# Kernel tuning notes

Measured on AMD Instinct MI355X. Metric: run time of the kernel, lower is better.

## Reference

```python
import jax, jax.numpy as jnp
import numpy as np

B, HW, C, D = 8, 65536, 64, 64  # batch, seq (H*W), channels, d_model
H = W = 256


def setup_inputs() -> dict:
    key = jax.random.key(0)
    ks = jax.random.split(key, 16)
    s = lambda k, shape, scale=0.05: jax.random.normal(k, shape, dtype=jnp.float32) * scale
    return {
        "x": jax.random.normal(ks[0], (B, HW, C), dtype=jnp.float32),
        "freq_map": jax.random.uniform(ks[1], (B, 1, H, W), dtype=jnp.float32),
        # proj_in: Linear(C, D)
        "W_in": s(ks[2], (C, D)), "b_in": s(ks[3], (D,)),
        # SimplifiedMambaKernel: in_proj Linear(D, 2D)
        "W_ip": s(ks[4], (D, 2 * D)), "b_ip": s(ks[5], (2 * D,)),
        # depthwise Conv1d(D, D, k=3, padding=1, groups=D): weight [D,1,3]
        "conv_w": s(ks[6], (D, 1, 3)), "conv_b": s(ks[7], (D,)),
        # mamba out_proj Linear(D, D)
        "W_op": s(ks[8], (D, D)), "b_op": s(ks[9], (D,)),
        # gate_net: Linear(1,16) -> ReLU -> Linear(16,C) -> Sigmoid
        "W_g1": s(ks[10], (1, 16)), "b_g1": s(ks[11], (16,)),
        "W_g2": s(ks[12], (16, C)), "b_g2": s(ks[13], (C,)),
        # proj_out: Linear(D, C)
        "W_out": s(ks[14], (D, C)), "b_out": s(ks[15], (C,)),
    }


def _mamba_kernel(feat, W_ip, b_ip, conv_w, conv_b, W_op, b_op):
    # feat: [B, L, D]
    x_and_res = feat @ W_ip + b_ip                      # [B, L, 2D]
    x_branch, res_branch = jnp.split(x_and_res, 2, axis=-1)
    xb = jnp.transpose(x_branch, (0, 2, 1))             # [B, D, L]
    xb = jax.lax.conv_general_dilated(
        xb, conv_w, window_strides=(1,), padding=[(1, 1)],
        feature_group_count=conv_w.shape[0],
        dimension_numbers=("NCH", "OIH", "NCH"))
    xb = xb + conv_b[None, :, None]
    x_branch = jnp.transpose(xb, (0, 2, 1))             # [B, L, D]
    out = jax.nn.silu(x_branch) * jax.nn.silu(res_branch)
    return out @ W_op + b_op


def reference(x, freq_map, W_in, b_in, W_ip, b_ip, conv_w, conv_b,
              W_op, b_op, W_g1, b_g1, W_g2, b_g2, W_out, b_out):
    feat = x @ W_in + b_in                              # [B, L, D]
    feat = _mamba_kernel(feat, W_ip, b_ip, conv_w, conv_b, W_op, b_op)
    feat_out = feat @ W_out + b_out                     # [B, L, C]
    # freq_map [B,1,H,W] -> flatten(2).permute(0,2,1) -> [B, L, 1]
    freq_flat = freq_map.reshape(freq_map.shape[0], 1, -1).transpose(0, 2, 1)
    gate = jax.nn.sigmoid(jax.nn.relu(freq_flat @ W_g1 + b_g1) @ W_g2 + b_g2)
    return feat_out * gate
```

## Files before the change

### kernel.cpp

```cpp
#include <hip/hip_runtime.h>
#include <hip/hip_bf16.h>

#define L_SEQ 65536
#define TILE 64
#define TILES_PER_B 1024

typedef __attribute__((ext_vector_type(8))) short bf16x8;
typedef __attribute__((ext_vector_type(4))) short s16x4;
typedef __attribute__((ext_vector_type(4))) float f32x4;

#define WS_WFX   0
#define WS_W1R   24576
#define WS_W2T   32768
#define WS_WG2T  40960
#define WS_BX    43008
#define WS_BR    43264
#define WS_BC0   43520
#define WS_BC2   43776
#define WS_B2    44032

__device__ __forceinline__ short f2bf(float f) {
    __bf16 h = (__bf16)f;
    return __builtin_bit_cast(short, h);
}
__device__ __forceinline__ float fsigmoid(float x) {
    return __builtin_amdgcn_rcpf(1.0f + __builtin_amdgcn_exp2f(-1.44269504089f * x));
}

__global__ void prep_kernel(const float* __restrict__ W_in, const float* __restrict__ b_in,
                            const float* __restrict__ W_ip, const float* __restrict__ b_ip,
                            const float* __restrict__ conv_w, const float* __restrict__ conv_b,
                            const float* __restrict__ W_op, const float* __restrict__ b_op,
                            const float* __restrict__ W_g2,
                            const float* __restrict__ W_out, const float* __restrict__ b_out,
                            void* __restrict__ ws)
{
    short* wfx  = (short*)((char*)ws + WS_WFX);
    short* w1r  = (short*)((char*)ws + WS_W1R);
    short* w2t  = (short*)((char*)ws + WS_W2T);
    short* wg2t = (short*)((char*)ws + WS_WG2T);
    float* bx   = (float*)((char*)ws + WS_BX);
    float* br   = (float*)((char*)ws + WS_BR);
    float* bc0  = (float*)((char*)ws + WS_BC0);
    float* bc2  = (float*)((char*)ws + WS_BC2);
    float* b2   = (float*)((char*)ws + WS_B2);

    int tid = blockIdx.x * blockDim.x + threadIdx.x;
    if (tid < 12288) {
        int s = tid >> 12, rem = tid & 4095;
        int d = rem >> 6, c = rem & 63;
        float acc = 0.f;
        for (int e = 0; e < 64; ++e) acc += W_in[c*64 + e] * W_ip[e*128 + d];
        wfx[(s*64 + d)*64 + c] = f2bf(acc * conv_w[3*d + s]);
    } else if (tid < 16384) {
        int rem = tid - 12288; int d = rem >> 6, c = rem & 63;
        float acc = 0.f;
        for (int e = 0; e < 64; ++e) acc += W_in[c*64 + e] * W_ip[e*128 + 64 + d];
        w1r[d*64 + c] = f2bf(acc);
    } else if (tid < 20480) {
        int rem = tid - 16384; int cp = rem >> 6, d = rem & 63;
        float acc = 0.f;
        for (int e = 0; e < 64; ++e) acc += W_op[d*64 + e] * W_out[e*64 + cp];
        w2t[cp*64 + d] = f2bf(acc);
    } else if (tid < 21504) {
        int rem = tid - 20480; int c = rem >> 4, j = rem & 15;
        wg2t[c*16 + j] = f2bf(W_g2[j*64 + c]);
    } else if (tid < 21568) {
        int d = tid - 21504;
        float b1x = b_ip[d];
        for (int e = 0; e < 64; ++e) b1x += b_in[e] * W_ip[e*128 + d];
        bx[d] = b1x * (conv_w[3*d] + conv_w[3*d+1] + conv_w[3*d+2]) + conv_b[d];
    } else if (tid < 21632) {
        int d = tid - 21568;
        float s = b_ip[64 + d];
        for (int e = 0; e < 64; ++e) s += b_in[e] * W_ip[e*128 + 64 + d];
        br[d] = s;
    } else if (tid < 21696) {
        int d = tid - 21632;
        float b1x = b_ip[d];
        for (int e = 0; e < 64; ++e) b1x += b_in[e] * W_ip[e*128 + d];
        bc0[d] = b1x * conv_w[3*d];
    } else if (tid < 21760) {
        int d = tid - 21696;
        float b1x = b_ip[d];
        for (int e = 0; e < 64; ++e) b1x += b_in[e] * W_ip[e*128 + d];
        bc2[d] = b1x * conv_w[3*d + 2];
    } else if (tid < 21824) {
        int cp = tid - 21760;
        float s = b_out[cp];
        for (int e = 0; e < 64; ++e) s += b_op[e] * W_out[e*64 + cp];
        b2[cp] = s;
    }
}

__global__ __launch_bounds__(256, 6) void fgs_main(
    const float* __restrict__ x, const float* __restrict__ freq,
    const float* __restrict__ wg1, const float* __restrict__ bg1,
    const float* __restrict__ bg2,
    const void* __restrict__ ws, float* __restrict__ out)
{
    const short* wfx  = (const short*)((const char*)ws + WS_WFX);
    const short* w1r  = (const short*)((const char*)ws + WS_W1R);
    const short* w2t  = (const short*)((const char*)ws + WS_W2T);
    const short* wg2t = (const short*)((const char*)ws + WS_WG2T);
    const float* bxv  = (const float*)((const char*)ws + WS_BX);
    const float* brv  = (const float*)((const char*)ws + WS_BR);
    const float* bc0  = (const float*)((const char*)ws + WS_BC0);
    const float* bc2  = (const float*)((const char*)ws + WS_BC2);
    const float* b2   = (const float*)((const char*)ws + WS_B2);

    __shared__ short xs[66 * 64];
    __shared__ short ot[64][72];
    __shared__ short hl[64][16];

    const int bid   = blockIdx.x;
    const int batch = bid >> 10;
    const int tile  = bid & 1023;
    const int base  = tile << 6;
    const bool edge = (tile == 0) || (tile == 1023);

    const int lane = threadIdx.x & 63;
    const int w    = threadIdx.x >> 6;
    const int lr   = lane & 15;
    const int g    = lane >> 4;
    const int r    = 16*w + lr;

    const size_t brow0 = (size_t)batch * L_SEQ;

    {
        auto stage_row = [&](int i, int cf) {
            int grow = base - 1 + i;
            bool v = ((unsigned)grow < (unsigned)L_SEQ);
            const float* p = x + (brow0 + (size_t)(v ? grow : 0)) * 64 + cf;
            float4 a = *(const float4*)(p);
            float4 b = *(const float4*)(p + 4);
            float4 c = *(const float4*)(p + 8);
            float4 d = *(const float4*)(p + 12);
            bf16x8 lo, hi;
            lo[0]=f2bf(a.x); lo[1]=f2bf(a.y); lo[2]=f2bf(a.z); lo[3]=f2bf(a.w);
            lo[4]=f2bf(b.x); lo[5]=f2bf(b.y); lo[6]=f2bf(b.z); lo[7]=f2bf(b.w);
            hi[0]=f2bf(c.x); hi[1]=f2bf(c.y); hi[2]=f2bf(c.z); hi[3]=f2bf(c.w);
            hi[4]=f2bf(d.x); hi[5]=f2bf(d.y); hi[6]=f2bf(d.z); hi[7]=f2bf(d.w);
            if (!v) { bf16x8 z = {}; lo = z; hi = z; }
            int c0 = cf >> 3;
            int sw = i & 7;
            *(bf16x8*)&xs[i*64 + ((c0    ) ^ sw) * 8] = lo;
            *(bf16x8*)&xs[i*64 + ((c0 + 1) ^ sw) * 8] = hi;
        };
        stage_row(threadIdx.x >> 2, (threadIdx.x & 3) * 16);
        if (threadIdx.x < 8)
            stage_row(64 + (threadIdx.x >> 2), (threadIdx.x & 3) * 16);
    }

    if (g < 2) {
        float f = freq[brow0 + base + r];
        float4 wa = *(const float4*)(wg1 + 8*g);
        float4 wb = *(const float4*)(wg1 + 8*g + 4);
        float4 ba = *(const float4*)(bg1 + 8*g);
        float4 bb = *(const float4*)(bg1 + 8*g + 4);
        bf16x8 hv;
        hv[0] = f2bf(fmaxf(f*wa.x + ba.x, 0.f));
        hv[1] = f2bf(fmaxf(f*wa.y + ba.y, 0.f));
        hv[2] = f2bf(fmaxf(f*wa.z + ba.z, 0.f));
        hv[3] = f2bf(fmaxf(f*wa.w + ba.w, 0.f));
        hv[4] = f2bf(fmaxf(f*wb.x + bb.x, 0.f));
        hv[5] = f2bf(fmaxf(f*wb.y + bb.y, 0.f));
        hv[6] = f2bf(fmaxf(f*wb.z + bb.z, 0.f));
        hv[7] = f2bf(fmaxf(f*wb.w + bb.w, 0.f));
        *(bf16x8*)&hl[r][8*g] = hv;
    }
    __syncthreads();

    f32x4 accx[4] = {};
    f32x4 accr[4] = {};
    #pragma unroll
    for (int kk = 0; kk < 2; ++kk) {
        #pragma unroll
        for (int s = 0; s < 3; ++s) {
            bf16x8 a = *(const bf16x8*)(wfx + (s*64 + 16*w + lr)*64 + 32*kk + 8*g);
            int rb = lr + s;
            const short* bp = xs + rb*64 + (((4*kk + g) ^ (rb & 7)) * 8);
            bf16x8 b0 = *(const bf16x8*)(bp);
            bf16x8 b1 = *(const bf16x8*)(bp + 1024);
            bf16x8 b2f = *(const bf16x8*)(bp + 2048);
            bf16x8 b3 = *(const bf16x8*)(bp + 3072);
            accx[0] = __builtin_amdgcn_mfma_f32_16x16x32_bf16(a, b0, accx[0], 0, 0, 0);
            accx[1] = __builtin_amdgcn_mfma_f32_16x16x32_bf16(a, b1, accx[1], 0, 0, 0);
            accx[2] = __builtin_amdgcn_mfma_f32_16x16x32_bf16(a, b2f, accx[2], 0, 0, 0);
            accx[3] = __builtin_amdgcn_mfma_f32_16x16x32_bf16(a, b3, accx[3], 0, 0, 0);
            if (s == 1) {
                bf16x8 ar = *(const bf16x8*)(w1r + (16*w + lr)*64 + 32*kk + 8*g);
                accr[0] = __builtin_amdgcn_mfma_f32_16x16x32_bf16(ar, b0, accr[0], 0, 0, 0);
                accr[1] = __builtin_amdgcn_mfma_f32_16x16x32_bf16(ar, b1, accr[1], 0, 0, 0);
                accr[2] = __builtin_amdgcn_mfma_f32_16x16x32_bf16(ar, b2f, accr[2], 0, 0, 0);
                accr[3] = __builtin_amdgcn_mfma_f32_16x16x32_bf16(ar, b3, accr[3], 0, 0, 0);
            }
        }
    }

    {
        const int c0 = 16*w + 4*g;
        float4 bbx = *(const float4*)(bxv + c0);
        float4 bbr = *(const float4*)(brv + c0);
        #pragma unroll
        for (int nt = 0; nt < 4; ++nt) {
            int trow = 16*nt + lr;
            f32x4 vx = accx[nt];
            f32x4 vr = accr[nt];
            vx[0] += bbx.x; vx[1] += bbx.y; vx[2] += bbx.z; vx[3] += bbx.w;
            vr[0] += bbr.x; vr[1] += bbr.y; vr[2] += bbr.z; vr[3] += bbr.w;
            if (edge) {
                int grow = base + trow;
                if (grow == 0) {
                    float4 c = *(const float4*)(bc0 + c0);
                    vx[0] -= c.x; vx[1] -= c.y; vx[2] -= c.z; vx[3] -= c.w;
                }
                if (grow == L_SEQ - 1) {
                    float4 c = *(const float4*)(bc2 + c0);
                    vx[0] -= c.x; vx[1] -= c.y; vx[2] -= c.z; vx[3] -= c.w;
                }
            }
            s16x4 pv;
            #pragma unroll
            for (int j = 0; j < 4; ++j) {
                float xx = vx[j], rr = vr[j];
                float ex = __builtin_amdgcn_exp2f(-1.44269504089f * xx);
                float er = __builtin_amdgcn_exp2f(-1.44269504089f * rr);
                float o = xx * rr * __builtin_amdgcn_rcpf((1.0f + ex) * (1.0f + er));
                pv[j] = f2bf(o);
            }
            *(s16x4*)&ot[trow][c0] = pv;
        }
    }
    __syncthreads();

    f32x4 acc2[4] = {};
    {
        bf16x8 a2_0 = *(const bf16x8*)(w2t + (16*w + lr)*64 + 8*g);
        bf16x8 a2_1 = *(const bf16x8*)(w2t + (16*w + lr)*64 + 32 + 8*g);
        #pragma unroll
        for (int nt = 0; nt < 4; ++nt) {
            int row = 16*nt + lr;
            bf16x8 bo0 = *(bf16x8*)&ot[row][8*g];
            bf16x8 bo1 = *(bf16x8*)&ot[row][32 + 8*g];
            acc2[nt] = __builtin_amdgcn_mfma_f32_16x16x32_bf16(a2_0, bo0, acc2[nt], 0, 0, 0);
            acc2[nt] = __builtin_amdgcn_mfma_f32_16x16x32_bf16(a2_1, bo1, acc2[nt], 0, 0, 0);
        }
    }
    f32x4 accg[4] = {};
    {
        bf16x8 zf = {};
        bf16x8 ag = (g < 2) ? *(const bf16x8*)(wg2t + (16*w + lr)*16 + 8*g) : zf;
        #pragma unroll
        for (int nt = 0; nt < 4; ++nt) {
            bf16x8 bh = (g < 2) ? *(bf16x8*)&hl[16*nt + lr][8*g] : zf;
            accg[nt] = __builtin_amdgcn_mfma_f32_16x16x32_bf16(ag, bh, accg[nt], 0, 0, 0);
        }
    }

    {
        const int c0 = 16*w + 4*g;
        float4 bb2 = *(const float4*)(b2 + c0);
        float4 bbg = *(const float4*)(bg2 + c0);
        float* op0 = out + (brow0 + (size_t)(base + lr)) * 64 + c0;
        #pragma unroll
        for (int nt = 0; nt < 4; ++nt) {
            f32x4 y = acc2[nt], gg = accg[nt];
            float4 o;
            o.x = (y[0] + bb2.x) * fsigmoid(gg[0] + bbg.x);
            o.y = (y[1] + bb2.y) * fsigmoid(gg[1] + bbg.y);
            o.z = (y[2] + bb2.z) * fsigmoid(gg[2] + bbg.z);
            o.w = (y[3] + bb2.w) * fsigmoid(gg[3] + bbg.w);
            *(float4*)(op0 + (size_t)(16*nt)*64) = o;
        }
    }
}

extern "C" void kernel_launch(void* const* d_in, const int* in_sizes, int n_in,
                              void* d_out, int out_size, void* d_ws, size_t ws_size,
                              hipStream_t stream)
{
    const float* x      = (const float*)d_in[0];
    const float* freq   = (const float*)d_in[1];
    const float* W_in   = (const float*)d_in[2];
    const float* b_in   = (const float*)d_in[3];
    const float* W_ip   = (const float*)d_in[4];
    const float* b_ip   = (const float*)d_in[5];
    const float* conv_w = (const float*)d_in[6];
    const float* conv_b = (const float*)d_in[7];
    const float* W_op   = (const float*)d_in[8];
    const float* b_op   = (const float*)d_in[9];
    const float* W_g1   = (const float*)d_in[10];
    const float* b_g1   = (const float*)d_in[11];
    const float* W_g2   = (const float*)d_in[12];
    const float* b_g2   = (const float*)d_in[13];
    const float* W_out  = (const float*)d_in[14];
    const float* b_out  = (const float*)d_in[15];
    float* out = (float*)d_out;

    prep_kernel<<<86, 256, 0, stream>>>(W_in, b_in, W_ip, b_ip, conv_w, conv_b,
                                        W_op, b_op, W_g2, W_out, b_out, d_ws);
    fgs_main<<<8 * TILES_PER_B, 256, 0, stream>>>(x, freq, W_g1, b_g1, b_g2, d_ws, out);
}
```

Before: 86.53 us.

## Process four tiles per block with double-buffered staging and register-resident weights

Each block now handles four consecutive 64-row tiles instead of one, keeping the conv/in-proj weight fragments in registers across tiles. Global loads of the next tile's x and freq are issued before the current tile's MFMAs and written to a second LDS buffer afterwards, and the halo rows are copied from the previous buffer instead of reloaded. This targets load latency, repeated weight fetches and halo reloads, at the cost of more registers, doubled LDS (occupancy bound lowered to 4) and fewer, longer blocks.

```diff
diff --git a/kernel.cpp b/kernel.cpp
--- a/kernel.cpp
+++ b/kernel.cpp
@@ -2,8 +2,7 @@
 #include <hip/hip_bf16.h>
 
 #define L_SEQ 65536
-#define TILE 64
-#define TILES_PER_B 1024
+#define GROUPS_PER_B 256
 
 typedef __attribute__((ext_vector_type(8))) short bf16x8;
 typedef __attribute__((ext_vector_type(4))) short s16x4;
@@ -93,7 +92,7 @@
     }
 }
 
-__global__ __launch_bounds__(256, 6) void fgs_main(
+__global__ __launch_bounds__(256, 4) void fgs_main(
     const float* __restrict__ x, const float* __restrict__ freq,
     const float* __restrict__ wg1, const float* __restrict__ bg1,
     const float* __restrict__ bg2,
@@ -109,99 +108,142 @@
     const float* bc2  = (const float*)((const char*)ws + WS_BC2);
     const float* b2   = (const float*)((const char*)ws + WS_B2);
 
-    __shared__ short xs[66 * 64];
+    __shared__ short xs[2][66 * 64];
     __shared__ short ot[64][72];
-    __shared__ short hl[64][16];
+    __shared__ short hl[2][64 * 16];
 
     const int bid   = blockIdx.x;
-    const int batch = bid >> 10;
-    const int tile  = bid & 1023;
-    const int base  = tile << 6;
-    const bool edge = (tile == 0) || (tile == 1023);
+    const int batch = bid >> 8;
+    const int tg    = bid & 255;
+    const int base0 = tg << 8;
 
     const int lane = threadIdx.x & 63;
     const int w    = threadIdx.x >> 6;
     const int lr   = lane & 15;
     const int g    = lane >> 4;
     const int r    = 16*w + lr;
+    const int c0   = 16*w + 4*g;
 
     const size_t brow0 = (size_t)batch * L_SEQ;
 
-    {
-        auto stage_row = [&](int i, int cf) {
-            int grow = base - 1 + i;
-            bool v = ((unsigned)grow < (unsigned)L_SEQ);
-            const float* p = x + (brow0 + (size_t)(v ? grow : 0)) * 64 + cf;
-            float4 a = *(const float4*)(p);
-            float4 b = *(const float4*)(p + 4);
-            float4 c = *(const float4*)(p + 8);
-            float4 d = *(const float4*)(p + 12);
-            bf16x8 lo, hi;
-            lo[0]=f2bf(a.x); lo[1]=f2bf(a.y); lo[2]=f2bf(a.z); lo[3]=f2bf(a.w);
-            lo[4]=f2bf(b.x); lo[5]=f2bf(b.y); lo[6]=f2bf(b.z); lo[7]=f2bf(b.w);
-            hi[0]=f2bf(c.x); hi[1]=f2bf(c.y); hi[2]=f2bf(c.z); hi[3]=f2bf(c.w);
-            hi[4]=f2bf(d.x); hi[5]=f2bf(d.y); hi[6]=f2bf(d.z); hi[7]=f2bf(d.w);
-            if (!v) { bf16x8 z = {}; lo = z; hi = z; }
-            int c0 = cf >> 3;
-            int sw = i & 7;
-            *(bf16x8*)&xs[i*64 + ((c0    ) ^ sw) * 8] = lo;
-            *(bf16x8*)&xs[i*64 + ((c0 + 1) ^ sw) * 8] = hi;
-        };
-        stage_row(threadIdx.x >> 2, (threadIdx.x & 3) * 16);
-        if (threadIdx.x < 8)
-            stage_row(64 + (threadIdx.x >> 2), (threadIdx.x & 3) * 16);
-    }
-
-    if (g < 2) {
-        float f = freq[brow0 + base + r];
-        float4 wa = *(const float4*)(wg1 + 8*g);
-        float4 wb = *(const float4*)(wg1 + 8*g + 4);
-        float4 ba = *(const float4*)(bg1 + 8*g);
-        float4 bb = *(const float4*)(bg1 + 8*g + 4);
-        bf16x8 hv;
-        hv[0] = f2bf(fmaxf(f*wa.x + ba.x, 0.f));
-        hv[1] = f2bf(fmaxf(f*wa.y + ba.y, 0.f));
-        hv[2] = f2bf(fmaxf(f*wa.z + ba.z, 0.f));
-        hv[3] = f2bf(fmaxf(f*wa.w + ba.w, 0.f));
-        hv[4] = f2bf(fmaxf(f*wb.x + bb.x, 0.f));
-        hv[5] = f2bf(fmaxf(f*wb.y + bb.y, 0.f));
-        hv[6] = f2bf(fmaxf(f*wb.z + bb.z, 0.f));
-        hv[7] = f2bf(fmaxf(f*wb.w + bb.w, 0.f));
-        *(bf16x8*)&hl[r][8*g] = hv;
-    }
-    __syncthreads();
-
-    f32x4 accx[4] = {};
-    f32x4 accr[4] = {};
+    bf16x8 awf[2][3], awr[2];
     #pragma unroll
     for (int kk = 0; kk < 2; ++kk) {
         #pragma unroll
-        for (int s = 0; s < 3; ++s) {
-            bf16x8 a = *(const bf16x8*)(wfx + (s*64 + 16*w + lr)*64 + 32*kk + 8*g);
-            int rb = lr + s;
-            const short* bp = xs + rb*64 + (((4*kk + g) ^ (rb & 7)) * 8);
-            bf16x8 b0 = *(const bf16x8*)(bp);
-            bf16x8 b1 = *(const bf16x8*)(bp + 1024);
-            bf16x8 b2f = *(const bf16x8*)(bp + 2048);
-            bf16x8 b3 = *(const bf16x8*)(bp + 3072);
-            accx[0] = __builtin_amdgcn_mfma_f32_16x16x32_bf16(a, b0, accx[0], 0, 0, 0);
-            accx[1] = __builtin_amdgcn_mfma_f32_16x16x32_bf16(a, b1, accx[1], 0, 0, 0);
-            accx[2] = __builtin_amdgcn_mfma_f32_16x16x32_bf16(a, b2f, accx[2], 0, 0, 0);
-            accx[3] = __builtin_amdgcn_mfma_f32_16x16x32_bf16(a, b3, accx[3], 0, 0, 0);
-            if (s == 1) {
-                bf16x8 ar = *(const bf16x8*)(w1r + (16*w + lr)*64 + 32*kk + 8*g);
-                accr[0] = __builtin_amdgcn_mfma_f32_16x16x32_bf16(ar, b0, accr[0], 0, 0, 0);
-                accr[1] = __builtin_amdgcn_mfma_f32_16x16x32_bf16(ar, b1, accr[1], 0, 0, 0);
-                accr[2] = __builtin_amdgcn_mfma_f32_16x16x32_bf16(ar, b2f, accr[2], 0, 0, 0);
-                accr[3] = __builtin_amdgcn_mfma_f32_16x16x32_bf16(ar, b3, accr[3], 0, 0, 0);
-            }
-        }
+        for (int s = 0; s < 3; ++s)
+            awf[kk][s] = *(const bf16x8*)(wfx + (s*64 + 16*w + lr)*64 + 32*kk + 8*g);
+        awr[kk] = *(const bf16x8*)(w1r + (16*w + lr)*64 + 32*kk + 8*g);
     }
-
-    {
-        const int c0 = 16*w + 4*g;
-        float4 bbx = *(const float4*)(bxv + c0);
-        float4 bbr = *(const float4*)(brv + c0);
+    const float4 bbx = *(const float4*)(bxv + c0);
+    const float4 bbr = *(const float4*)(brv + c0);
+    const float4 wgv = *(const float4*)(wg1 + 4*g);
+    const float4 bgv = *(const float4*)(bg1 + 4*g);
+
+    float4 sa, sb, sc, sd; float sf;
+    const int sro = threadIdx.x >> 2;
+    const int sq  = (threadIdx.x & 3) * 16;
+
+    auto stage_issue = [&](int tb) {
+        int grow = tb + 1 + sro;
+        bool v = ((unsigned)grow < (unsigned)L_SEQ);
+        const float* p = x + (brow0 + (size_t)(v ? grow : 0)) * 64 + sq;
+        sa = *(const float4*)(p);
+        sb = *(const float4*)(p + 4);
+        sc = *(const float4*)(p + 8);
+        sd = *(const float4*)(p + 12);
+        sf = freq[brow0 + tb + r];
+    };
+    auto stage_write = [&](short* xb, int tb) {
+        int i = 2 + sro;
+        int grow = tb + 1 + sro;
+        bool v = ((unsigned)grow < (unsigned)L_SEQ);
+        bf16x8 lo, hi;
+        lo[0]=f2bf(sa.x); lo[1]=f2bf(sa.y); lo[2]=f2bf(sa.z); lo[3]=f2bf(sa.w);
+        lo[4]=f2bf(sb.x); lo[5]=f2bf(sb.y); lo[6]=f2bf(sb.z); lo[7]=f2bf(sb.w);
+        hi[0]=f2bf(sc.x); hi[1]=f2bf(sc.y); hi[2]=f2bf(sc.z); hi[3]=f2bf(sc.w);
+        hi[4]=f2bf(sd.x); hi[5]=f2bf(sd.y); hi[6]=f2bf(sd.z); hi[7]=f2bf(sd.w);
+        if (!v) { bf16x8 z = {}; lo = z; hi = z; }
+        int cb = sq >> 3;
+        int sw = i & 7;
+        *(bf16x8*)&xb[i*64 + ((cb    ) ^ sw) * 8] = lo;
+        *(bf16x8*)&xb[i*64 + ((cb + 1) ^ sw) * 8] = hi;
+    };
+    auto halo_copy = [&](short* xb, const short* xprev) {
+        if (threadIdx.x < 16) {
+            int ii = threadIdx.x >> 3;
+            int cc = threadIdx.x & 7;
+            *(bf16x8*)&xb[ii*64 + cc*8] = *(const bf16x8*)&xprev[(64 + ii)*64 + cc*8];
+        }
+    };
+    auto hl_write = [&](short* hb) {
+        s16x4 hv;
+        hv[0] = f2bf(fmaxf(sf*wgv.x + bgv.x, 0.f));
+        hv[1] = f2bf(fmaxf(sf*wgv.y + bgv.y, 0.f));
+        hv[2] = f2bf(fmaxf(sf*wgv.z + bgv.z, 0.f));
+        hv[3] = f2bf(fmaxf(sf*wgv.w + bgv.w, 0.f));
+        *(s16x4*)&hb[r*16 + 4*g] = hv;
+    };
+
+    stage_issue(base0);
+    if (threadIdx.x < 8) {
+        int i = threadIdx.x >> 2;
+        int grow = base0 - 1 + i;
+        bool v = (grow >= 0);
+        const float* p = x + (brow0 + (size_t)(v ? grow : 0)) * 64 + sq;
+        float4 a = *(const float4*)(p);
+        float4 b = *(const float4*)(p + 4);
+        float4 c = *(const float4*)(p + 8);
+        float4 d = *(const float4*)(p + 12);
+        bf16x8 lo, hi;
+        lo[0]=f2bf(a.x); lo[1]=f2bf(a.y); lo[2]=f2bf(a.z); lo[3]=f2bf(a.w);
+        lo[4]=f2bf(b.x); lo[5]=f2bf(b.y); lo[6]=f2bf(b.z); lo[7]=f2bf(b.w);
+        hi[0]=f2bf(c.x); hi[1]=f2bf(c.y); hi[2]=f2bf(c.z); hi[3]=f2bf(c.w);
+        hi[4]=f2bf(d.x); hi[5]=f2bf(d.y); hi[6]=f2bf(d.z); hi[7]=f2bf(d.w);
+        if (!v) { bf16x8 z = {}; lo = z; hi = z; }
+        int cb = sq >> 3;
+        int sw = i & 7;
+        *(bf16x8*)&xs[0][i*64 + ((cb    ) ^ sw) * 8] = lo;
+        *(bf16x8*)&xs[0][i*64 + ((cb + 1) ^ sw) * 8] = hi;
+    }
+    stage_write(xs[0], base0);
+    hl_write(hl[0]);
+    __syncthreads();
+
+    #pragma unroll
+    for (int t = 0; t < 4; ++t) {
+        const int tb = base0 + (t << 6);
+        short* xcur = xs[t & 1];
+        short* xnxt = xs[(t & 1) ^ 1];
+        short* hcur = hl[t & 1];
+        short* hnxt = hl[(t & 1) ^ 1];
+
+        if (t < 3) stage_issue(tb + 64);
+
+        f32x4 accx[4] = {};
+        f32x4 accr[4] = {};
+        #pragma unroll
+        for (int kk = 0; kk < 2; ++kk) {
+            #pragma unroll
+            for (int s = 0; s < 3; ++s) {
+                int rb = lr + s;
+                const short* bp = xcur + rb*64 + (((4*kk + g) ^ (rb & 7)) * 8);
+                bf16x8 b0 = *(const bf16x8*)(bp);
+                bf16x8 b1v = *(const bf16x8*)(bp + 1024);
+                bf16x8 b2v = *(const bf16x8*)(bp + 2048);
+                bf16x8 b3v = *(const bf16x8*)(bp + 3072);
+                accx[0] = __builtin_amdgcn_mfma_f32_16x16x32_bf16(awf[kk][s], b0,  accx[0], 0, 0, 0);
+                accx[1] = __builtin_amdgcn_mfma_f32_16x16x32_bf16(awf[kk][s], b1v, accx[1], 0, 0, 0);
+                accx[2] = __builtin_amdgcn_mfma_f32_16x16x32_bf16(awf[kk][s], b2v, accx[2], 0, 0, 0);
+                accx[3] = __builtin_amdgcn_mfma_f32_16x16x32_bf16(awf[kk][s], b3v, accx[3], 0, 0, 0);
+                if (s == 1) {
+                    accr[0] = __builtin_amdgcn_mfma_f32_16x16x32_bf16(awr[kk], b0,  accr[0], 0, 0, 0);
+                    accr[1] = __builtin_amdgcn_mfma_f32_16x16x32_bf16(awr[kk], b1v, accr[1], 0, 0, 0);
+                    accr[2] = __builtin_amdgcn_mfma_f32_16x16x32_bf16(awr[kk], b2v, accr[2], 0, 0, 0);
+                    accr[3] = __builtin_amdgcn_mfma_f32_16x16x32_bf16(awr[kk], b3v, accr[3], 0, 0, 0);
+                }
+            }
+        }
+
         #pragma unroll
         for (int nt = 0; nt < 4; ++nt) {
             int trow = 16*nt + lr;
@@ -209,16 +251,13 @@
             f32x4 vr = accr[nt];
             vx[0] += bbx.x; vx[1] += bbx.y; vx[2] += bbx.z; vx[3] += bbx.w;
             vr[0] += bbr.x; vr[1] += bbr.y; vr[2] += bbr.z; vr[3] += bbr.w;
-            if (edge) {
-                int grow = base + trow;
-                if (grow == 0) {
-                    float4 c = *(const float4*)(bc0 + c0);
-                    vx[0] -= c.x; vx[1] -= c.y; vx[2] -= c.z; vx[3] -= c.w;
-                }
-                if (grow == L_SEQ - 1) {
-                    float4 c = *(const float4*)(bc2 + c0);
-                    vx[0] -= c.x; vx[1] -= c.y; vx[2] -= c.z; vx[3] -= c.w;
-                }
+            if (t == 0 && nt == 0 && tg == 0 && lr == 0) {
+                float4 cc = *(const float4*)(bc0 + c0);
+                vx[0] -= cc.x; vx[1] -= cc.y; vx[2] -= cc.z; vx[3] -= cc.w;
+            }
+            if (t == 3 && nt == 3 && tg == 255 && lr == 15) {
+                float4 cc = *(const float4*)(bc2 + c0);
+                vx[0] -= cc.x; vx[1] -= cc.y; vx[2] -= cc.z; vx[3] -= cc.w;
             }
             s16x4 pv;
             #pragma unroll
@@ -231,48 +270,47 @@
             }
             *(s16x4*)&ot[trow][c0] = pv;
         }
-    }
-    __syncthreads();
-
-    f32x4 acc2[4] = {};
-    {
+        __syncthreads();
+
+        if (t < 3) {
+            stage_write(xnxt, tb + 64);
+            halo_copy(xnxt, xcur);
+            hl_write(hnxt);
+        }
+
         bf16x8 a2_0 = *(const bf16x8*)(w2t + (16*w + lr)*64 + 8*g);
         bf16x8 a2_1 = *(const bf16x8*)(w2t + (16*w + lr)*64 + 32 + 8*g);
+        bf16x8 zf = {};
+        bf16x8 ag = (g < 2) ? *(const bf16x8*)(wg2t + (16*w + lr)*16 + 8*g) : zf;
+        f32x4 acc2[4] = {};
+        f32x4 accg[4] = {};
         #pragma unroll
         for (int nt = 0; nt < 4; ++nt) {
             int row = 16*nt + lr;
             bf16x8 bo0 = *(bf16x8*)&ot[row][8*g];
             bf16x8 bo1 = *(bf16x8*)&ot[row][32 + 8*g];
+            bf16x8 bh  = (g < 2) ? *(bf16x8*)&hcur[row*16 + 8*g] : zf;
             acc2[nt] = __builtin_amdgcn_mfma_f32_16x16x32_bf16(a2_0, bo0, acc2[nt], 0, 0, 0);
             acc2[nt] = __builtin_amdgcn_mfma_f32_16x16x32_bf16(a2_1, bo1, acc2[nt], 0, 0, 0);
-        }
-    }
-    f32x4 accg[4] = {};
-    {
-        bf16x8 zf = {};
-        bf16x8 ag = (g < 2) ? *(const bf16x8*)(wg2t + (16*w + lr)*16 + 8*g) : zf;
-        #pragma unroll
-        for (int nt = 0; nt < 4; ++nt) {
-            bf16x8 bh = (g < 2) ? *(bf16x8*)&hl[16*nt + lr][8*g] : zf;
-            accg[nt] = __builtin_amdgcn_mfma_f32_16x16x32_bf16(ag, bh, accg[nt], 0, 0, 0);
-        }
-    }
-
-    {
-        const int c0 = 16*w + 4*g;
-        float4 bb2 = *(const float4*)(b2 + c0);
-        float4 bbg = *(const float4*)(bg2 + c0);
-        float* op0 = out + (brow0 + (size_t)(base + lr)) * 64 + c0;
-        #pragma unroll
-        for (int nt = 0; nt < 4; ++nt) {
-            f32x4 y = acc2[nt], gg = accg[nt];
-            float4 o;
-            o.x = (y[0] + bb2.x) * fsigmoid(gg[0] + bbg.x);
-            o.y = (y[1] + bb2.y) * fsigmoid(gg[1] + bbg.y);
-            o.z = (y[2] + bb2.z) * fsigmoid(gg[2] + bbg.z);
-            o.w = (y[3] + bb2.w) * fsigmoid(gg[3] + bbg.w);
-            *(float4*)(op0 + (size_t)(16*nt)*64) = o;
-        }
+            accg[nt] = __builtin_amdgcn_mfma_f32_16x16x32_bf16(ag,   bh,  accg[nt], 0, 0, 0);
+        }
+
+        {
+            float4 bb2 = *(const float4*)(b2 + c0);
+            float4 bbg = *(const float4*)(bg2 + c0);
+            float* op0 = out + (brow0 + (size_t)(tb + lr)) * 64 + c0;
+            #pragma unroll
+            for (int nt = 0; nt < 4; ++nt) {
+                f32x4 y = acc2[nt], gg = accg[nt];
+                float4 o;
+                o.x = (y[0] + bb2.x) * fsigmoid(gg[0] + bbg.x);
+                o.y = (y[1] + bb2.y) * fsigmoid(gg[1] + bbg.y);
+                o.z = (y[2] + bb2.z) * fsigmoid(gg[2] + bbg.z);
+                o.w = (y[3] + bb2.w) * fsigmoid(gg[3] + bbg.w);
+                *(float4*)(op0 + (size_t)(nt << 4) * 64) = o;
+            }
+        }
+        if (t < 3) __syncthreads();
     }
 }
 
@@ -300,5 +338,5 @@
 
     prep_kernel<<<86, 256, 0, stream>>>(W_in, b_in, W_ip, b_ip, conv_w, conv_b,
                                         W_op, b_op, W_g2, W_out, b_out, d_ws);
-    fgs_main<<<8 * TILES_PER_B, 256, 0, stream>>>(x, freq, W_g1, b_g1, b_g2, d_ws, out);
-}
+    fgs_main<<<8 * GROUPS_PER_B, 256, 0, stream>>>(x, freq, W_g1, b_g1, b_g2, d_ws, out);
+}
```

New measurement: 95.47 us. +10.3%, slower.
